# Kernel optimization log

Hardware: AMD Instinct MI355X
Metric: run time of the kernel (lower is better)

## Reference

```python
import math
import jax, jax.numpy as jnp
import numpy as np

B, N, W, D, H = 16, 64, 128, 128, 4

def posenc(L, d):
    pos = jnp.arange(L, dtype=jnp.float32)[:, None]
    div = jnp.exp(jnp.arange(0, d, 2, dtype=jnp.float32) * (-math.log(10000.0) / d))
    pe = jnp.zeros((L, d), jnp.float32)
    pe = pe.at[:, 0::2].set(jnp.sin(pos * div))
    pe = pe.at[:, 1::2].set(jnp.cos(pos * div))
    return pe

def ln(x):
    # torch nn.LayerNorm(x.shape[1:]) created fresh each call: normalize over all non-batch dims, no affine
    ax = tuple(range(1, x.ndim))
    m = x.mean(ax, keepdims=True)
    v = ((x - m) ** 2).mean(ax, keepdims=True)
    return (x - m) / jnp.sqrt(v + 1e-5)

def conv1d(x, w, b):
    # x [B,C,L], w [Cout,Cin,K] (torch layout), VALID padding
    y = jax.lax.conv_general_dilated(x, w, (1,), 'VALID', dimension_numbers=('NCH', 'OIH', 'NCH'))
    return y + b[None, :, None]

def convt1d(x, w, b, stride, pad):
    # torch ConvTranspose1d, w [Cin,Cout,K]
    K = w.shape[2]
    w_ = jnp.flip(w, 2).transpose(1, 0, 2)  # [Cout,Cin,K]
    y = jax.lax.conv_general_dilated(x, w_, (1,), [(K - 1 - pad, K - 1 - pad)],
                                     lhs_dilation=(stride,), dimension_numbers=('NCH', 'OIH', 'NCH'))
    return y + b[None, :, None]

def mha(q, k, v, wi, bi, wo, bo):
    # torch nn.MultiheadAttention(batch_first=True), H heads
    d = q.shape[-1]
    qp = q @ wi[:d].T + bi[:d]
    kp = k @ wi[d:2 * d].T + bi[d:2 * d]
    vp = v @ wi[2 * d:].T + bi[2 * d:]
    def heads(t):
        b_, l_, _ = t.shape
        return t.reshape(b_, l_, H, d // H).transpose(0, 2, 1, 3)
    qh, kh, vh = heads(qp), heads(kp), heads(vp)
    s = jnp.einsum('bhqd,bhkd->bhqk', qh, kh) / jnp.sqrt(jnp.asarray(d // H, qh.dtype))
    o = jnp.einsum('bhqk,bhkd->bhqd', jax.nn.softmax(s, -1), vh)
    b_, l_ = q.shape[0], q.shape[1]
    return o.transpose(0, 2, 1, 3).reshape(b_, l_, d) @ wo.T + bo


def setup_inputs():
    key = jax.random.key(0)
    ks = iter(jax.random.split(key, 64))
    def w(shape, s=0.05):
        return jax.random.normal(next(ks), shape, jnp.float32) * s
    inp = {}
    inp['tokens'] = jax.random.randint(next(ks), (B, N, W), 0, 257, jnp.int32)
    inp['emb_table'] = w((257, D), 1.0)
    for nm in ['ce', 'ct', 'cg', 'ces', 'cts']:
        inp['w_' + nm] = w((D, D, 3))
        inp['b_' + nm] = w((D,))
    inp['mha_wi'] = w((3 * D, D)); inp['mha_bi'] = w((3 * D,))
    inp['mha_wo'] = w((D, D)); inp['mha_bo'] = w((D,))
    s = 1.0 / math.sqrt(D)
    inp['tgt1'] = jax.random.uniform(next(ks), (1, D), jnp.float32, -s, s)
    inp['tgt2'] = jax.random.uniform(next(ks), (1, D), jnp.float32, -s, s)
    for nm in ['mu', 'lv', 'di']:
        inp['w_' + nm] = w((D, D)); inp['b_' + nm] = w((D,))
    inp['eps'] = jax.random.normal(next(ks), (B, D), jnp.float32)
    inp['dk_w'] = w((32, 32)); inp['dk_b'] = w((32,))
    inp['dv_w'] = w((32, 32)); inp['dv_b'] = w((32,))
    inp['wt1'] = w((32, 64, 3)); inp['bt1'] = w((64,))
    inp['wt2'] = w((64, 128, 3)); inp['bt2'] = w((128,))
    for nm in ['sq', 'sk', 'sv']:
        inp[nm + '_w'] = w((128, 128)); inp[nm + '_b'] = w((128,))
    inp['wt3'] = w((128, 128, 3)); inp['bt3'] = w((128,))
    return inp


def reference(tokens, emb_table, w_ce, b_ce, w_ct, b_ct, w_cg, b_cg, w_ces, b_ces, w_cts, b_cts,
              mha_wi, mha_bi, mha_wo, mha_bo, tgt1, tgt2,
              w_mu, b_mu, w_lv, b_lv, w_di, b_di, eps,
              dk_w, dk_b, dv_w, dv_b, wt1, bt1, wt2, bt2,
              sq_w, sq_b, sk_w, sk_b, sv_w, sv_b, wt3, bt3):
    emb = emb_table[tokens] + posenc(W, D)                    # [B,N,W,D]
    flat = emb.reshape(B * N, W, D)                           # batch the per-sample torch loop

    def word_branch(wc, bc, act):
        h = act(conv1d(flat.transpose(0, 2, 1), wc, bc)).transpose(0, 2, 1)  # [BN,W-2,D]
        return mha(h, h, h, mha_wi, mha_bi, mha_wo, mha_bo)

    a_e = jax.nn.elu(word_branch(w_ce, b_ce, jax.nn.elu))
    a_t = jnp.tanh(word_branch(w_ct, b_ct, jnp.tanh))
    xw = ln((a_e * a_t).reshape(B, N, W - 2, D)).reshape(B * N, W - 2, D)

    h = jax.nn.elu(conv1d(xw.transpose(0, 2, 1), w_cg, b_cg)).transpose(0, 2, 1)  # [BN,W-4,D]
    q1 = jnp.broadcast_to(tgt1[None], (B * N, 1, D))
    out = mha(q1, h, h, mha_wi, mha_bi, mha_wo, mha_bo)[:, 0, :].reshape(B, N, D)

    se = out + posenc(N, D)                                   # sentence level

    def sent_branch(wc, bc, act):
        hh = act(conv1d(se.transpose(0, 2, 1), wc, bc)).transpose(0, 2, 1)       # [B,N-2,D]
        return mha(hh, hh, hh, mha_wi, mha_bi, mha_wo, mha_bo)

    s_e = jax.nn.elu(sent_branch(w_ces, b_ces, jax.nn.elu))
    s_t = jnp.tanh(sent_branch(w_cts, b_cts, jnp.tanh))
    xs = ln(s_e * s_t)
    q2 = jnp.broadcast_to(tgt2[None], (B, 1, D))
    doc = mha(q2, xs, xs, mha_wi, mha_bi, mha_wo, mha_bo)[:, 0, :]

    mu = doc @ w_mu.T + b_mu
    lv = doc @ w_lv.T + b_lv
    z = mu + eps * jnp.exp(0.5 * lv)

    h = (z @ w_di.T + b_di).reshape(B, 32, -1)                # [B,32,4]
    L = h.shape[2]
    k = jnp.einsum('oi,bil->bol', dk_w, h) + dk_b[None, :, None]
    v = jnp.einsum('oi,bil->bol', dv_w, h) + dv_b[None, :, None]
    kh = k.reshape(B, H, 8, L)
    vh = v.reshape(B, H, 8, L)
    att = jax.nn.softmax(jnp.einsum('bhdl,bhdm->bhlm', kh, vh) / jnp.sqrt(8.0), -1)
    h = jax.nn.elu(jnp.einsum('bhlm,bhdm->bhld', att, vh).reshape(B, 32, L))
    h = jax.nn.elu(ln(convt1d(h, wt1, bt1, 2, 1)))            # [B,64,7]
    h = jax.nn.elu(ln(convt1d(h, wt2, bt2, 2, 1)))            # [B,128,13]
    L2 = h.shape[2]
    qc = jnp.einsum('oi,bil->bol', sq_w, h) + sq_b[None, :, None]
    kc = jnp.einsum('oi,bil->bol', sk_w, h) + sk_b[None, :, None]
    vc = jnp.einsum('oi,bil->bol', sv_w, h) + sv_b[None, :, None]
    qh = qc.reshape(B, H, 32, L2)
    khh = kc.reshape(B, H, 32, L2)
    att = jax.nn.softmax(jnp.einsum('bhdl,bhdm->bhlm', qh, khh) / jnp.sqrt(32.0), -1)
    vr = vc.reshape(B, H, 32, L2).reshape(B, H, L2, 32)       # faithful torch .view reinterpretation
    h = jax.nn.elu(jnp.einsum('bhlm,bhmd->bhld', att, vr).reshape(B, 128, L2))
    recon = jax.nn.sigmoid(ln(convt1d(h, wt3, bt3, 1, 1)))    # [B,128,13]
    return recon, mu, lv
```

## Files before the change

### kernel.cpp

```cpp
#include <hip/hip_runtime.h>
#include <hip/hip_bf16.h>

typedef __hip_bfloat16 bf16;
typedef __attribute__((ext_vector_type(8))) short bf16x8;
typedef __attribute__((ext_vector_type(4))) float f32x4;

__device__ __forceinline__ float b2f(bf16 x){ return __bfloat162float(x); }
__device__ __forceinline__ bf16  f2b(float x){ return __float2bfloat16(x); }
__device__ __forceinline__ unsigned short b2u(bf16 x){ union{bf16 b; unsigned short u;} c; c.b = x; return c.u; }

#define LOG2E 1.4426950408889634f
#define QSC (0.17677669529663687f * LOG2E)

#define GLD16(gp, lp) __builtin_amdgcn_global_load_lds( \
    (const __attribute__((address_space(1))) void*)(gp), \
    (__attribute__((address_space(3))) void*)(lp), 16, 0, 0)

__device__ __forceinline__ float fexp2(float x){
  float r; asm("v_exp_f32 %0, %1" : "=v"(r) : "v"(x)); return r;
}
__device__ __forceinline__ float fast_exp(float x){ return fexp2(x * LOG2E); }
__device__ __forceinline__ float eluf(float x){ return x > 0.f ? x : fast_exp(x) - 1.f; }
__device__ __forceinline__ float fast_tanh(float x){
  float cx = fminf(fmaxf(x, -15.f), 15.f);
  float t = fexp2(cx * (2.f*LOG2E));
  return (t - 1.f) / (t + 1.f);
}

#define PE_C (-0.07195578415606394f)

__device__ __forceinline__ float pe_val(int pos, int d){
  int j2 = d & ~1;
  float ang = (float)pos * expf((float)j2 * PE_C);
  return (d & 1) ? cosf(ang) : sinf(ang);
}

__device__ __forceinline__ void pack_one(const float* __restrict__ W, bf16* __restrict__ out,
                                         int K, int N, int conv, int qscale, int t){
  int j = t & 7, lane = (t >> 3) & 63;
  int rest = t >> 9; int NT = N >> 4;
  int nt = rest % NT; int kb = rest / NT;
  int k = kb*32 + ((lane >> 4) << 3) + j;
  int n = nt*16 + (lane & 15);
  float v = conv ? W[n*384 + (k & 127)*3 + (k >> 7)] : W[(long)n*K + k];
  if (qscale && n < 128) v *= QSC;
  out[t] = f2b(v);
}

__global__ void k_prep(const float* __restrict__ w_ce, const float* __restrict__ w_ct,
                       const float* __restrict__ w_cg, const float* __restrict__ w_ces,
                       const float* __restrict__ w_cts, const float* __restrict__ wi,
                       const float* __restrict__ wo,
                       bf16* P_CE, bf16* P_CT, bf16* P_CG, bf16* P_CES, bf16* P_CTS,
                       bf16* P_WI, bf16* P_WO, float* __restrict__ pet){
  int bid = blockIdx.x;
  if (bid < 1152){
    int grp = bid / 192; int t = (bid % 192)*256 + threadIdx.x;
    const float* W; bf16* out; int K, N, conv, qs = 0;
    if      (grp == 0){ W = w_ce;  out = P_CE;  K=384; N=128; conv=1; }
    else if (grp == 1){ W = w_ct;  out = P_CT;  K=384; N=128; conv=1; }
    else if (grp == 2){ W = w_cg;  out = P_CG;  K=384; N=128; conv=1; }
    else if (grp == 3){ W = w_ces; out = P_CES; K=384; N=128; conv=1; }
    else if (grp == 4){ W = w_cts; out = P_CTS; K=384; N=128; conv=1; }
    else              { W = wi;    out = P_WI;  K=128; N=384; conv=0; qs=1; }
    pack_one(W, out, K, N, conv, qs, t);
  } else if (bid < 1216){
    int t = (bid - 1152)*256 + threadIdx.x;
    pack_one(wo, P_WO, 128, 128, 0, 0, t);
  } else {
    int i = (bid - 1216)*256 + threadIdx.x;
    if (i < 16384) pet[i] = pe_val(i >> 7, i & 127);
  }
}

__global__ void k_qprep(const float* __restrict__ wi, const float* __restrict__ bi,
                        const float* __restrict__ t1, const float* __restrict__ t2,
                        float* __restrict__ rkv){
  int tid = threadIdx.x;
  __shared__ float qps[256];
  {
    int which = tid >> 7, jj = tid & 127;
    const float* t = which ? t2 : t1;
    float a = bi[jj];
    for (int i = 0; i < 128; ++i) a += wi[jj*128 + i] * t[i];
    qps[tid] = a;
  }
  __syncthreads();
  int i = tid & 127, which = tid >> 7;
  for (int h = 0; h < 4; ++h){
    float a = 0.f;
    for (int d = 0; d < 32; ++d) a += qps[which*128 + h*32 + d] * wi[(128 + h*32 + d)*128 + i];
    rkv[which*512 + h*128 + i] = a;
  }
}

template<bool GLL>
__global__ __launch_bounds__(256)
void k_gemm_mfma(const bf16* __restrict__ A, const bf16* __restrict__ Bp_, const bf16* __restrict__ Bp2,
                 const float* __restrict__ bias_, const float* __restrict__ bias2,
                 bf16* __restrict__ C_, bf16* __restrict__ C2p,
                 const bf16* __restrict__ mul,
                 int M, int K, int a_lout, int a_lind, int lda,
                 int NT, int n0t, int ldc, int act_, int act2,
                 const float* __restrict__ lnst, int lngrp,
                 const int* __restrict__ tok, const float* __restrict__ tabp,
                 const float* __restrict__ petp, const float* __restrict__ sepe,
                 float* __restrict__ part){
  const bf16* Bp = Bp_; const float* bias = bias_; bf16* C = C_; int act = act_;
  if (blockIdx.z){ Bp = Bp2; bias = bias2; C = C2p; act = act2; }

  __shared__ f32x4 AsV[2][512];
  __shared__ float redp[16];
  char* As0 = (char*)AsV[0];
  char* As1 = (char*)AsV[1];
  int tid = threadIdx.x;
  int lane = tid & 63, wave = tid >> 6;
  int wm = wave >> 1, wn = wave & 1;
  int m0 = blockIdx.x*128;
  int by = blockIdx.y;

  long offA[2]; bool okA[2]; float lnm[2], lnr[2]; int sbyte[2];
  #pragma unroll
  for (int p = 0; p < 2; ++p){
    int e = tid + p*256;
    int row, kq;
    if (GLL){
      int x = e;
      row = (((x >> 3) << 1) | (((x >> 2) ^ (x >> 4)) & 1)) & 127;
      kq  = ((((x >> 1) ^ (x >> 3)) & 1) << 1) | ((x ^ (x >> 2) ^ (x >> 4)) & 1);
    } else {
      row = e >> 2; kq = e & 3;
    }
    int m = m0 + row;
    okA[p] = (m < M);
    long off = 0;
    if (okA[p]){
      off = (a_lout > 0) ? (long)(m / a_lout)*a_lind + (long)(m % a_lout)*128 + kq*8
                         : (long)m*lda + kq*8;
    }
    offA[p] = off;
    lnm[p] = 0.f; lnr[p] = 1.f;
    if (!GLL && lnst && okA[p]){ int g = (int)(off / (long)lngrp); lnm[p] = lnst[2*g]; lnr[p] = lnst[2*g+1]; }
    sbyte[p] = (row*64 + kq*16) ^ ((row & 7) << 4);
  }

  const bf16* bptr[4];
  size_t bstep = (size_t)NT*512;
  #pragma unroll
  for (int fn = 0; fn < 4; ++fn){
    int ntile = n0t + by*8 + wn*4 + fn;
    bptr[fn] = Bp + ((size_t)ntile*64 + lane)*8;
  }
  int abyte[4];
  #pragma unroll
  for (int fm = 0; fm < 4; ++fm){
    int row = wm*64 + fm*16 + (lane & 15);
    abyte[fm] = (row*64 + ((lane >> 4) << 4)) ^ ((row & 7) << 4);
  }

  f32x4 acc[4][4];
  #pragma unroll
  for (int i = 0; i < 4; ++i)
    #pragma unroll
    for (int j = 0; j < 4; ++j) acc[i][j] = (f32x4){0.f,0.f,0.f,0.f};

  int nk = K >> 5;

  if constexpr (GLL){
    int ldsw = (tid >> 6)*1024;
    #pragma unroll
    for (int p = 0; p < 2; ++p)
      GLD16(A + offA[p], As0 + p*4096 + ldsw);
    __syncthreads();
    for (int kb = 0; kb < nk; ++kb){
      char* cur = (kb & 1) ? As1 : As0;
      char* nxt = (kb & 1) ? As0 : As1;
      bool more = (kb + 1) < nk;
      if (more){
        #pragma unroll
        for (int p = 0; p < 2; ++p)
          GLD16(A + offA[p] + (kb+1)*32, nxt + p*4096 + ldsw);
      }
      bf16x8 bfr[4];
      #pragma unroll
      for (int fn = 0; fn < 4; ++fn) bfr[fn] = *(const bf16x8*)(bptr[fn] + (size_t)kb*bstep);
      bf16x8 afr[4];
      #pragma unroll
      for (int fm = 0; fm < 4; ++fm) afr[fm] = *(const bf16x8*)(cur + abyte[fm]);
      #pragma unroll
      for (int fm = 0; fm < 4; ++fm)
        #pragma unroll
        for (int fn = 0; fn < 4; ++fn)
          acc[fm][fn] = __builtin_amdgcn_mfma_f32_16x16x32_bf16(afr[fm], bfr[fn], acc[fm][fn], 0, 0, 0);
      __syncthreads();
    }
  } else {
    auto loadA = [&](int p, int kb)->float4{
      float4 v = make_float4(0.f,0.f,0.f,0.f);
      if (okA[p]){
        long e = offA[p] + kb*32;
        if (tok){
          int seq = (int)(e >> 14); int rest = (int)e & 16383;
          int wrow = rest >> 7, d0 = rest & 127;
          int t = tok[(seq << 7) + wrow];
          const float* ta = tabp + t*128 + d0;
          const float* pe = petp + (wrow << 7) + d0;
          bf16 oo[8];
          #pragma unroll
          for (int u = 0; u < 8; ++u) oo[u] = f2b(ta[u] + pe[u]);
          v = *(float4*)&oo[0];
        } else {
          v = *(const float4*)(A + e);
          if (lnst){
            bf16* pp = (bf16*)&v; bf16 oo[8];
            #pragma unroll
            for (int u = 0; u < 8; ++u) oo[u] = f2b((b2f(pp[u]) - lnm[p]) * lnr[p]);
            v = *(float4*)&oo[0];
          }
        }
      }
      return v;
    };
    float4 va0 = loadA(0, 0), va1 = loadA(1, 0);
    *(float4*)(As0 + sbyte[0]) = va0;
    *(float4*)(As0 + sbyte[1]) = va1;
    __syncthreads();
    for (int kb = 0; kb < nk; ++kb){
      char* cur = (kb & 1) ? As1 : As0;
      char* nxt = (kb & 1) ? As0 : As1;
      bool more = (kb + 1) < nk;
      if (more){ va0 = loadA(0, kb+1); va1 = loadA(1, kb+1); }
      bf16x8 bfr[4];
      #pragma unroll
      for (int fn = 0; fn < 4; ++fn) bfr[fn] = *(const bf16x8*)(bptr[fn] + (size_t)kb*bstep);
      bf16x8 afr[4];
      #pragma unroll
      for (int fm = 0; fm < 4; ++fm) afr[fm] = *(const bf16x8*)(cur + abyte[fm]);
      #pragma unroll
      for (int fm = 0; fm < 4; ++fm)
        #pragma unroll
        for (int fn = 0; fn < 4; ++fn)
          acc[fm][fn] = __builtin_amdgcn_mfma_f32_16x16x32_bf16(afr[fm], bfr[fn], acc[fm][fn], 0, 0, 0);
      if (more){
        *(float4*)(nxt + sbyte[0]) = va0;
        *(float4*)(nxt + sbyte[1]) = va1;
      }
      __syncthreads();
    }
  }

  float ps = 0.f, ps2 = 0.f;
  #pragma unroll
  for (int fm = 0; fm < 4; ++fm){
    #pragma unroll
    for (int r = 0; r < 4; ++r){
      int m = m0 + wm*64 + fm*16 + ((lane >> 4) << 2) + r;
      if (m >= M) continue;
      #pragma unroll
      for (int fn = 0; fn < 4; ++fn){
        int n = by*128 + wn*64 + fn*16 + (lane & 15);
        float v = acc[fm][fn][r] + (bias ? bias[n] : 0.f);
        if (act == 1) v = eluf(v);
        else if (act == 2) v = fast_tanh(v);
        if (mul) v *= b2f(mul[(long)m*ldc + n]);
        if (sepe) v += sepe[(m & 63)*128 + n];
        if (part){ ps += v; ps2 += v*v; }
        C[(long)m*ldc + n] = f2b(v);
      }
    }
  }
  if (part){
    #pragma unroll
    for (int o = 32; o; o >>= 1){ ps += __shfl_xor(ps, o); ps2 += __shfl_xor(ps2, o); }
    if (lane == 0){ redp[wave] = ps; redp[8 + wave] = ps2; }
    __syncthreads();
    if (tid == 0){
      part[blockIdx.x*2]     = redp[0]+redp[1]+redp[2]+redp[3];
      part[blockIdx.x*2 + 1] = redp[8]+redp[9]+redp[10]+redp[11];
    }
  }
}

template<int L>
__global__ __launch_bounds__(256)
void k_attn_fused(const bf16* __restrict__ X, const bf16* __restrict__ Pwi,
                  const float* __restrict__ bi, bf16* __restrict__ o){
  constexpr int KB  = (L + 31) / 32;
  constexpr int MT  = KB * 2;
  constexpr int WMT = MT / 4;
  constexpr int NP  = KB * 32;
  constexpr int PRS = NP * 2;

  __shared__ alignas(16) char As[NP*256];
  __shared__ alignas(16) char Qb[NP*64];
  __shared__ alignas(16) char Kb[NP*64];
  __shared__ alignas(16) char Vt[32*PRS];
  char* Pb = As;

  int tid = threadIdx.x;
  int s = blockIdx.x >> 2, h = blockIdx.x & 3;
  const bf16* xb = X + (size_t)s*L*128;

  {
    constexpr int NCH = (NP*16)/256;
    int ldsw = (tid >> 6)*1024;
    #pragma unroll
    for (int p = 0; p < NCH; ++p){
      int x = p*256 + tid;
      int row = x >> 4;
      int c = (x & 15) ^ (row & 7);
      const bf16* gp = (row < L) ? (xb + (size_t)row*128 + c*8) : xb;
      GLD16(gp, As + p*4096 + ldsw);
    }
  }
  __syncthreads();

  int lane = tid & 63, wave = tid >> 6;
  int col = lane & 15;

  __builtin_amdgcn_s_setprio(1);
  #pragma unroll
  for (int mt = 0; mt < WMT; ++mt){
    int mtile = wave*WMT + mt;
    int arow = mtile*16 + col;
    bf16x8 a4[4];
    #pragma unroll
    for (int kb = 0; kb < 4; ++kb)
      a4[kb] = *(const bf16x8*)(As + ((arow*256 + kb*64 + ((lane >> 4) << 4)) ^ ((arow & 7) << 4)));
    #pragma unroll
    for (int which = 0; which < 3; ++which){
      f32x4 av[2];
      #pragma unroll
      for (int nt = 0; nt < 2; ++nt){
        int ntile = which*8 + h*2 + nt;
        float bia = bi[which*128 + h*32 + nt*16 + col];
        if (which == 0) bia *= QSC;
        av[nt] = (f32x4){bia, bia, bia, bia};
        #pragma unroll
        for (int kb = 0; kb < 4; ++kb){
          bf16x8 bfr = *(const bf16x8*)(Pwi + (((size_t)kb*24 + ntile)*64 + lane)*8);
          av[nt] = __builtin_amdgcn_mfma_f32_16x16x32_bf16(a4[kb], bfr, av[nt], 0, 0, 0);
        }
      }
      #pragma unroll
      for (int r = 0; r < 4; ++r){
        int row = mtile*16 + ((lane >> 4) << 2) + r;
        if (which < 2){
          unsigned pk = (unsigned)b2u(f2b(av[0][r])) | ((unsigned)b2u(f2b(av[1][r])) << 16);
          char* dst = which ? Kb : Qb;
          *(unsigned*)(dst + ((row*64 + col*4) ^ ((row & 7) << 4))) = pk;
        } else {
          int pos = (row & 15)*MT + (row >> 4);
          #pragma unroll
          for (int nt = 0; nt < 2; ++nt){
            int d = nt*16 + col;
            *(bf16*)(Vt + ((d*PRS + pos*2) ^ ((d & 7) << 4))) = f2b(av[nt][r]);
          }
        }
      }
    }
  }
  __builtin_amdgcn_s_setprio(0);
  __syncthreads();

  f32x4 acc[WMT][MT];
  #pragma unroll
  for (int mt = 0; mt < WMT; ++mt)
    #pragma unroll
    for (int nt = 0; nt < MT; ++nt) acc[mt][nt] = (f32x4){0.f,0.f,0.f,0.f};

  bf16x8 af[WMT];
  #pragma unroll
  for (int mt = 0; mt < WMT; ++mt){
    int row = (wave*WMT + mt)*16 + col;
    af[mt] = *(const bf16x8*)(Qb + ((row*64 + ((lane >> 4) << 4)) ^ ((row & 7) << 4)));
  }
  __builtin_amdgcn_s_setprio(1);
  #pragma unroll
  for (int nt = 0; nt < MT; ++nt){
    int rk2 = nt*16 + col;
    bf16x8 bfk = *(const bf16x8*)(Kb + ((rk2*64 + ((lane >> 4) << 4)) ^ ((rk2 & 7) << 4)));
    #pragma unroll
    for (int mt = 0; mt < WMT; ++mt)
      acc[mt][nt] = __builtin_amdgcn_mfma_f32_16x16x32_bf16(af[mt], bfk, acc[mt][nt], 0, 0, 0);
  }
  __builtin_amdgcn_s_setprio(0);

  const bool lastMask = col >= (L - (MT-1)*16);
  float pinv[WMT][4];
  #pragma unroll
  for (int mt = 0; mt < WMT; ++mt){
    #pragma unroll
    for (int r = 0; r < 4; ++r){
      float mx = -1e30f;
      #pragma unroll
      for (int nt = 0; nt < MT; ++nt){
        float v = acc[mt][nt][r];
        if (nt == MT-1 && lastMask){ v = -1e30f; acc[mt][nt][r] = v; }
        mx = fmaxf(mx, v);
      }
      mx = fmaxf(mx, __shfl_xor(mx, 1));
      mx = fmaxf(mx, __shfl_xor(mx, 2));
      mx = fmaxf(mx, __shfl_xor(mx, 4));
      mx = fmaxf(mx, __shfl_xor(mx, 8));
      float sum = 0.f;
      bf16 prow[MT];
      #pragma unroll
      for (int nt = 0; nt < MT; ++nt){
        float p = fexp2(acc[mt][nt][r] - mx);
        prow[nt] = f2b(p);
        sum += p;
      }
      sum += __shfl_xor(sum, 1);
      sum += __shfl_xor(sum, 2);
      sum += __shfl_xor(sum, 4);
      sum += __shfl_xor(sum, 8);
      pinv[mt][r] = 1.f / sum;
      int row = (wave*WMT + mt)*16 + ((lane >> 4) << 2) + r;
      char* dst = Pb + ((row*PRS + col*(MT*2)) ^ ((row & 7) << 4));
      if constexpr (MT == 8) *(f32x4*)dst = *(f32x4*)prow;
      else                   *(float2*)dst = *(float2*)prow;
    }
  }

  #pragma unroll
  for (int mt = 0; mt < WMT; ++mt){
    int mtile = wave*WMT + mt;
    f32x4 o0 = (f32x4){0.f,0.f,0.f,0.f}, o1 = (f32x4){0.f,0.f,0.f,0.f};
    __builtin_amdgcn_s_setprio(1);
    #pragma unroll
    for (int kb = 0; kb < KB; ++kb){
      int row = mtile*16 + col;
      bf16x8 pa = *(const bf16x8*)(Pb + ((row*PRS + kb*64 + ((lane >> 4) << 4)) ^ ((row & 7) << 4)));
      int d0 = col;
      bf16x8 v0 = *(const bf16x8*)(Vt + ((d0*PRS + kb*64 + ((lane >> 4) << 4)) ^ ((d0 & 7) << 4)));
      bf16x8 v1 = *(const bf16x8*)(Vt + (((d0+16)*PRS + kb*64 + ((lane >> 4) << 4)) ^ (((d0+16) & 7) << 4)));
      o0 = __builtin_amdgcn_mfma_f32_16x16x32_bf16(pa, v0, o0, 0, 0, 0);
      o1 = __builtin_amdgcn_mfma_f32_16x16x32_bf16(pa, v1, o1, 0, 0, 0);
    }
    __builtin_amdgcn_s_setprio(0);
    #pragma unroll
    for (int r = 0; r < 4; ++r){
      int row = mtile*16 + ((lane >> 4) << 2) + r;
      if (row < L){
        size_t ob = ((size_t)s*L + row)*128 + h*32 + col;
        o[ob]      = f2b(o0[r] * pinv[mt][r]);
        o[ob + 16] = f2b(o1[r] * pinv[mt][r]);
      }
    }
  }
}

template<int L>
__global__ __launch_bounds__(256)
void k_attn_tgt(const bf16* __restrict__ hin, const float* __restrict__ rk,
                const float* __restrict__ wi, const float* __restrict__ bi,
                bf16* __restrict__ outp){
  __shared__ alignas(16) char Hs[L*256];
  __shared__ float RKs[512];
  __shared__ float Ps[512];
  __shared__ float Cs[512];
  int tid = threadIdx.x, lane = tid & 63, wave = tid >> 6;
  int s = blockIdx.x;
  const bf16* hb = hin + (size_t)s*L*128;
  for (int e = tid; e < L*16; e += 256){
    int row = e >> 4, c = e & 15;
    *(float4*)(Hs + row*256 + ((c ^ (row & 7)) << 4)) = *(const float4*)(hb + row*128 + c*8);
  }
  for (int e = tid; e < 512; e += 256) RKs[e] = rk[e];
  __syncthreads();

  int j0 = lane, j1 = lane + 64;
  float v0 = -1e30f, v1 = -1e30f;
  if (j0 < L){
    float a = 0.f;
    #pragma unroll
    for (int c = 0; c < 16; ++c){
      bf16x8 x = *(const bf16x8*)(Hs + j0*256 + ((c ^ (j0 & 7)) << 4));
      #pragma unroll
      for (int u = 0; u < 8; ++u) a += b2f(((bf16*)&x)[u]) * RKs[wave*128 + c*8 + u];
    }
    v0 = a * 0.17677669529663687f;
  }
  if (j1 < L){
    float a = 0.f;
    #pragma unroll
    for (int c = 0; c < 16; ++c){
      bf16x8 x = *(const bf16x8*)(Hs + j1*256 + ((c ^ (j1 & 7)) << 4));
      #pragma unroll
      for (int u = 0; u < 8; ++u) a += b2f(((bf16*)&x)[u]) * RKs[wave*128 + c*8 + u];
    }
    v1 = a * 0.17677669529663687f;
  }
  float mx = fmaxf(v0, v1);
  #pragma unroll
  for (int off = 32; off; off >>= 1) mx = fmaxf(mx, __shfl_xor(mx, off));
  float e0 = (j0 < L) ? fast_exp(v0 - mx) : 0.f;
  float e1 = (j1 < L) ? fast_exp(v1 - mx) : 0.f;
  float sum = e0 + e1;
  #pragma unroll
  for (int off = 32; off; off >>= 1) sum += __shfl_xor(sum, off);
  float inv = 1.f / sum;
  Ps[wave*128 + j0] = e0 * inv;
  Ps[wave*128 + j1] = e1 * inv;

  int i0 = lane*2;
  float c0 = 0.f, c1 = 0.f;
  for (int j = 0; j < L; ++j){
    float p = Ps[wave*128 + j];
    short2 w2 = *(const short2*)(Hs + j*256 + (((i0 >> 3) ^ (j & 7)) << 4) + (i0 & 7)*2);
    c0 += p * b2f(*(bf16*)&w2.x);
    c1 += p * b2f(*(bf16*)&w2.y);
  }
  Cs[wave*128 + i0]     = c0;
  Cs[wave*128 + i0 + 1] = c1;
  __syncthreads();

  if (tid < 128){
    int h2 = tid >> 5;
    float a = bi[256 + tid];
    const float* wr = wi + (size_t)(256 + tid)*128;
    for (int i = 0; i < 128; ++i) a += wr[i] * Cs[h2*128 + i];
    outp[(size_t)s*128 + tid] = f2b(a);
  }
}

__global__ void k_ln_fin(const float* __restrict__ part, float* __restrict__ stats, int P, int GS){
  int g = blockIdx.x;
  float s = 0.f, s2 = 0.f;
  for (int i = threadIdx.x; i < P; i += 256){ s += part[(g*P + i)*2]; s2 += part[(g*P + i)*2 + 1]; }
  #pragma unroll
  for (int off = 32; off; off >>= 1){ s += __shfl_xor(s, off); s2 += __shfl_xor(s2, off); }
  __shared__ float sh[8];
  int lane = threadIdx.x & 63, wv = threadIdx.x >> 6;
  if (lane == 0){ sh[wv] = s; sh[4 + wv] = s2; }
  __syncthreads();
  if (threadIdx.x == 0){
    float S = sh[0]+sh[1]+sh[2]+sh[3], S2 = sh[4]+sh[5]+sh[6]+sh[7];
    float mean = S / GS;
    float var = S2 / GS - mean*mean;
    stats[g*2] = mean; stats[g*2 + 1] = rsqrtf(var + 1e-5f);
  }
}

__global__ void k_ln_small_bf16(const bf16* __restrict__ x, bf16* __restrict__ y, int n){
  int g = blockIdx.x;
  const bf16* xb = x + (size_t)g*n;
  bf16* yb = y + (size_t)g*n;
  float s = 0.f, s2 = 0.f;
  for (int i = threadIdx.x; i < n; i += 256){ float v = b2f(xb[i]); s += v; s2 += v*v; }
  #pragma unroll
  for (int off = 32; off; off >>= 1){ s += __shfl_xor(s, off); s2 += __shfl_xor(s2, off); }
  __shared__ float sh[8];  __shared__ float ms[2];
  int lane = threadIdx.x & 63, wv = threadIdx.x >> 6;
  if (lane == 0){ sh[wv] = s; sh[4 + wv] = s2; }
  __syncthreads();
  if (threadIdx.x == 0){
    float S = sh[0]+sh[1]+sh[2]+sh[3], S2 = sh[4]+sh[5]+sh[6]+sh[7];
    float mean = S / n;
    ms[0] = mean; ms[1] = rsqrtf(S2 / n - mean*mean + 1e-5f);
  }
  __syncthreads();
  float mean = ms[0], inv = ms[1];
  for (int i = threadIdx.x; i < n; i += 256) yb[i] = f2b((b2f(xb[i]) - mean)*inv);
}

__global__ void k_ln_small_f32(const float* __restrict__ x, float* __restrict__ y, int n, int act){
  int g = blockIdx.x;
  const float* xb = x + (size_t)g*n;
  float* yb = y + (size_t)g*n;
  float s = 0.f, s2 = 0.f;
  for (int i = threadIdx.x; i < n; i += 256){ float v = xb[i]; s += v; s2 += v*v; }
  #pragma unroll
  for (int off = 32; off; off >>= 1){ s += __shfl_xor(s, off); s2 += __shfl_xor(s2, off); }
  __shared__ float sh[8];  __shared__ float ms[2];
  int lane = threadIdx.x & 63, wv = threadIdx.x >> 6;
  if (lane == 0){ sh[wv] = s; sh[4 + wv] = s2; }
  __syncthreads();
  if (threadIdx.x == 0){
    float S = sh[0]+sh[1]+sh[2]+sh[3], S2 = sh[4]+sh[5]+sh[6]+sh[7];
    float mean = S / n;
    ms[0] = mean; ms[1] = rsqrtf(S2 / n - mean*mean + 1e-5f);
  }
  __syncthreads();
  float mean = ms[0], inv = ms[1];
  for (int i = threadIdx.x; i < n; i += 256){
    float v = (xb[i] - mean)*inv;
    if (act == 1) v = eluf(v);
    else if (act == 3) v = 1.f/(1.f + fast_exp(-v));
    yb[i] = v;
  }
}

__global__ __launch_bounds__(256)
void k_dec_a(const bf16* __restrict__ DOC,
             const float* __restrict__ w_mu, const float* __restrict__ b_mu,
             const float* __restrict__ w_lv, const float* __restrict__ b_lv,
             const float* __restrict__ eps,
             const float* __restrict__ w_di, const float* __restrict__ b_di,
             const float* __restrict__ dk_w, const float* __restrict__ dk_b,
             const float* __restrict__ dv_w, const float* __restrict__ dv_b,
             const float* __restrict__ wt1, const float* __restrict__ bt1,
             float* __restrict__ dout, float* __restrict__ DEC2){
  int b = blockIdx.x, tid = threadIdx.x;
  __shared__ float Zs[128], H3[128], KD[128], VD[128], D1[128];
  __shared__ float C1[448];
  __shared__ float sc[64];
  __shared__ float red[8], ms[2];

  if (tid < 128){
    const bf16* dr = DOC + b*128;
    float mu = b_mu[tid], lv = b_lv[tid];
    for (int i = 0; i < 128; ++i){
      float x = b2f(dr[i]);
      mu += x * w_mu[tid*128 + i];
      lv += x * w_lv[tid*128 + i];
    }
    dout[26624 + b*128 + tid] = mu;
    dout[28672 + b*128 + tid] = lv;
    Zs[tid] = mu + eps[b*128 + tid] * fast_exp(0.5f*lv);
  }
  __syncthreads();
  if (tid < 128){
    float a = b_di[tid];
    for (int i = 0; i < 128; ++i) a += Zs[i] * w_di[tid*128 + i];
    H3[tid] = a;
  }
  __syncthreads();
  if (tid < 128){
    int l = tid & 3, o2 = tid >> 2;
    float ak = dk_b[o2], av = dv_b[o2];
    for (int i = 0; i < 32; ++i){
      float xv = H3[i*4 + l];
      ak += dk_w[o2*32 + i]*xv;
      av += dv_w[o2*32 + i]*xv;
    }
    KD[tid] = ak; VD[tid] = av;
  }
  __syncthreads();
  if (tid < 64){
    int h = tid >> 4, l = (tid >> 2) & 3, m = tid & 3;
    float a = 0.f;
    #pragma unroll
    for (int d = 0; d < 8; ++d) a += KD[(h*8+d)*4 + l] * VD[(h*8+d)*4 + m];
    sc[tid] = a * 0.35355339059327373f;
  }
  __syncthreads();
  if (tid < 16){
    int base = tid*4;
    float mx = fmaxf(fmaxf(sc[base],sc[base+1]),fmaxf(sc[base+2],sc[base+3]));
    float e0=fast_exp(sc[base]-mx), e1=fast_exp(sc[base+1]-mx), e2=fast_exp(sc[base+2]-mx), e3=fast_exp(sc[base+3]-mx);
    float inv = 1.f/(e0+e1+e2+e3);
    sc[base]=e0*inv; sc[base+1]=e1*inv; sc[base+2]=e2*inv; sc[base+3]=e3*inv;
  }
  __syncthreads();
  if (tid < 128){
    int h = tid >> 5, rem = tid & 31, l = rem >> 3, d = rem & 7;
    float a = 0.f;
    #pragma unroll
    for (int m = 0; m < 4; ++m) a += sc[h*16 + l*4 + m] * VD[(h*8+d)*4 + m];
    D1[tid] = eluf(a);
  }
  __syncthreads();
  for (int idx = tid; idx < 448; idx += 256){
    int co = idx / 7, lo = idx % 7;
    float a = bt1[co];
    for (int k = 0; k < 3; ++k){
      int t = lo + 1 - k;
      if (t < 0 || (t & 1)) continue;
      int li = t >> 1; if (li >= 4) continue;
      float aa = 0.f;
      for (int ci = 0; ci < 32; ++ci) aa += D1[ci*4 + li] * wt1[ci*192 + co*3 + k];
      a += aa;
    }
    C1[idx] = a;
  }
  __syncthreads();
  {
    float s = 0.f, s2 = 0.f;
    for (int i = tid; i < 448; i += 256){ float v = C1[i]; s += v; s2 += v*v; }
    #pragma unroll
    for (int o = 32; o; o >>= 1){ s += __shfl_xor(s, o); s2 += __shfl_xor(s2, o); }
    int lane = tid & 63, wv = tid >> 6;
    if (lane == 0){ red[wv] = s; red[4+wv] = s2; }
    __syncthreads();
    if (tid == 0){
      float S = red[0]+red[1]+red[2]+red[3], S2 = red[4]+red[5]+red[6]+red[7];
      float mean = S/448.f; ms[0] = mean; ms[1] = rsqrtf(S2/448.f - mean*mean + 1e-5f);
    }
    __syncthreads();
    float mean = ms[0], inv = ms[1];
    for (int i = tid; i < 448; i += 256)
      DEC2[b*448 + i] = eluf((C1[i]-mean)*inv);
  }
}

__global__ void k_chanproj3(const float* __restrict__ x,
                            const float* __restrict__ w1, const float* __restrict__ b1,
                            const float* __restrict__ w2, const float* __restrict__ b2,
                            const float* __restrict__ w3, const float* __restrict__ b3,
                            float* __restrict__ y1, float* __restrict__ y2, float* __restrict__ y3,
                            int Bn, int C, int L){
  int idx = blockIdx.x*256 + threadIdx.x;
  if (idx >= Bn*C*L) return;
  int l = idx % L; int t2 = idx / L; int o = t2 % C; int b = t2 / C;
  float a1 = b1[o], a2 = b2[o], a3 = b3[o];
  const float* xb = x + (size_t)b*C*L + l;
  for (int i = 0; i < C; ++i){
    float xv = xb[i*L];
    a1 += w1[(size_t)o*C + i]*xv;
    a2 += w2[(size_t)o*C + i]*xv;
    a3 += w3[(size_t)o*C + i]*xv;
  }
  y1[idx] = a1; y2[idx] = a2; y3[idx] = a3;
}

__global__ __launch_bounds__(256)
void k_dec_attn2(const float* __restrict__ qc, const float* __restrict__ kc,
                 const float* __restrict__ vc, float* __restrict__ out){
  int b = blockIdx.x >> 2, h = blockIdx.x & 3, tid = threadIdx.x;
  __shared__ float sc[169];
  const float* qb = qc + b*1664 + h*416;
  const float* kb = kc + b*1664 + h*416;
  const float* vb = vc + b*1664 + h*416;
  if (tid < 169){
    int l = tid/13, m = tid - l*13;
    float a = 0.f;
    #pragma unroll
    for (int d = 0; d < 32; ++d) a += qb[d*13 + l] * kb[d*13 + m];
    sc[tid] = a * 0.17677669529663687f;
  }
  __syncthreads();
  if (tid < 13){
    float mx = -1e30f;
    for (int m = 0; m < 13; ++m) mx = fmaxf(mx, sc[tid*13 + m]);
    float s = 0.f;
    for (int m = 0; m < 13; ++m){ float p = fast_exp(sc[tid*13 + m] - mx); sc[tid*13 + m] = p; s += p; }
    float inv = 1.f/s;
    for (int m = 0; m < 13; ++m) sc[tid*13 + m] *= inv;
  }
  __syncthreads();
  for (int idx = tid; idx < 416; idx += 256){
    int l = idx >> 5, d = idx & 31;
    float a = 0.f;
    for (int m = 0; m < 13; ++m) a += sc[l*13 + m] * vb[m*32 + d];
    out[b*1664 + h*416 + idx] = eluf(a);
  }
}

__global__ __launch_bounds__(256)
void k_convt(const float* __restrict__ x, const float* __restrict__ w,
             const float* __restrict__ bias, float* __restrict__ y,
             int Bn, int Ci, int Co, int Lin, int Lout, int stride, int pad, int nch){
  __shared__ float xs[1664];
  int b = blockIdx.x / nch;
  int c0 = (blockIdx.x % nch)*16;
  int tid = threadIdx.x;
  for (int i = tid; i < Ci*Lin; i += 256) xs[i] = x[(size_t)b*Ci*Lin + i];
  __syncthreads();
  int co = c0 + (tid & 15);
  int lo = tid >> 4;
  if (co >= Co || lo >= Lout) return;
  float a = bias[co];
  for (int k = 0; k < 3; ++k){
    int t = lo + pad - k;
    if (t < 0 || (t % stride)) continue;
    int li = t / stride;
    if (li >= Lin) continue;
    float aa = 0.f;
    for (int ci = 0; ci < Ci; ++ci) aa += xs[ci*Lin + li] * w[(size_t)ci*Co*3 + co*3 + k];
    a += aa;
  }
  y[(size_t)b*Co*Lout + co*Lout + lo] = a;
}

extern "C" void kernel_launch(void* const* d_in, const int* in_sizes, int n_in,
                              void* d_out, int out_size, void* d_ws, size_t ws_size,
                              hipStream_t stream){
  const int*   tokens = (const int*)  d_in[0];
  const float* tab    = (const float*)d_in[1];
  const float* w_ce = (const float*)d_in[2];  const float* b_ce = (const float*)d_in[3];
  const float* w_ct = (const float*)d_in[4];  const float* b_ct = (const float*)d_in[5];
  const float* w_cg = (const float*)d_in[6];  const float* b_cg = (const float*)d_in[7];
  const float* w_ces= (const float*)d_in[8];  const float* b_ces= (const float*)d_in[9];
  const float* w_cts= (const float*)d_in[10]; const float* b_cts= (const float*)d_in[11];
  const float* wi   = (const float*)d_in[12]; const float* bi   = (const float*)d_in[13];
  const float* wo   = (const float*)d_in[14]; const float* bo   = (const float*)d_in[15];
  const float* tgt1 = (const float*)d_in[16]; const float* tgt2 = (const float*)d_in[17];
  const float* w_mu = (const float*)d_in[18]; const float* b_mu = (const float*)d_in[19];
  const float* w_lv = (const float*)d_in[20]; const float* b_lv = (const float*)d_in[21];
  const float* w_di = (const float*)d_in[22]; const float* b_di = (const float*)d_in[23];
  const float* epsb = (const float*)d_in[24];
  const float* dk_w = (const float*)d_in[25]; const float* dk_b = (const float*)d_in[26];
  const float* dv_w = (const float*)d_in[27]; const float* dv_b = (const float*)d_in[28];
  const float* wt1  = (const float*)d_in[29]; const float* bt1  = (const float*)d_in[30];
  const float* wt2  = (const float*)d_in[31]; const float* bt2  = (const float*)d_in[32];
  const float* sq_w = (const float*)d_in[33]; const float* sq_b = (const float*)d_in[34];
  const float* sk_w = (const float*)d_in[35]; const float* sk_b = (const float*)d_in[36];
  const float* sv_w = (const float*)d_in[37]; const float* sv_b = (const float*)d_in[38];
  const float* wt3  = (const float*)d_in[39]; const float* bt3  = (const float*)d_in[40];

  float* dout = (float*)d_out;

  char* ws = (char*)d_ws;
  size_t off = 0;
  auto take = [&](size_t bytes)->char*{ char* p = ws + off; off += (bytes + 255) & ~(size_t)255; return p; };
  bf16* EMB  = (bf16*)take(16777216ull*2);
  bf16* HB   = (bf16*)take(16515072ull*2);
  bf16* OB   = (bf16*)take(16515072ull*2);
  bf16* AE   = (bf16*)take(16515072ull*2);
  bf16* O1   = (bf16*)take(131072ull*2);
  bf16* SEB  = (bf16*)take(131072ull*2);
  bf16* SH   = (bf16*)take(126976ull*2);
  bf16* SCT  = (bf16*)take(126976ull*2);
  bf16* SO   = (bf16*)take(126976ull*2);
  bf16* SAE  = (bf16*)take(126976ull*2);
  bf16* XS   = (bf16*)take(126976ull*2);
  bf16* DO1  = (bf16*)take(2048ull*2);
  bf16* DOC  = (bf16*)take(2048ull*2);
  float* RK  = (float*)take(1024*4);
  float* PART= (float*)take(1008ull*2*4);
  float* STATS=(float*)take(32*4);
  float* DEC2= (float*)take(7168*4);
  float* C2  = (float*)take(26624*4);
  float* DEC3= (float*)take(26624*4);
  float* QC  = (float*)take(26624*4);
  float* KC  = (float*)take(26624*4);
  float* VC  = (float*)take(26624*4);
  float* DEC4= (float*)take(26624*4);
  float* C3  = (float*)take(26624*4);
  float* PET = (float*)take(16384*4);
  bf16* P_CE = (bf16*)take(49152ull*2);
  bf16* P_CT = (bf16*)take(49152ull*2);
  bf16* P_CG = (bf16*)take(49152ull*2);
  bf16* P_CES= (bf16*)take(49152ull*2);
  bf16* P_CTS= (bf16*)take(49152ull*2);
  bf16* P_WI = (bf16*)take(49152ull*2);
  bf16* P_WO = (bf16*)take(16384ull*2);
  (void)ws_size; (void)in_sizes; (void)n_in; (void)out_size;

  auto cdiv = [](long a, long b){ return (int)((a + b - 1)/b); };
  auto gemm = [&](const bf16* A, const bf16* Bpp, const float* bias, bf16* C, const bf16* mul,
                  int M, int N, int K, int a_lout, int a_lind, int lda, int NT, int n0t, int ldc, int act,
                  const float* lnst, int lngrp, const float* sepe, float* part){
    dim3 g(cdiv(M,128), N/128, 1);
    if (lnst)
      k_gemm_mfma<false><<<g, 256, 0, stream>>>(A, Bpp, Bpp, bias, bias, C, C, mul,
                                                M, K, a_lout, a_lind, lda, NT, n0t, ldc, act, act, lnst, lngrp,
                                                nullptr, nullptr, nullptr, sepe, part);
    else
      k_gemm_mfma<true><<<g, 256, 0, stream>>>(A, Bpp, Bpp, bias, bias, C, C, mul,
                                               M, K, a_lout, a_lind, lda, NT, n0t, ldc, act, act, nullptr, 0,
                                               nullptr, nullptr, nullptr, sepe, part);
  };
  auto gemmz_emb = [&](const bf16* Bp1, const float* b1, bf16* C1, int act1,
                       const bf16* Bp2, const float* b2, bf16* C2p, int act2,
                       int M, int N, int K, int a_lout, int a_lind, int NT, int ldc){
    dim3 g(cdiv(M,128), N/128, 2);
    k_gemm_mfma<false><<<g, 256, 0, stream>>>(nullptr, Bp1, Bp2, b1, b2, C1, C2p, nullptr,
                                              M, K, a_lout, a_lind, 0, NT, 0, ldc, act1, act2, nullptr, 0,
                                              tokens, tab, PET, nullptr, nullptr);
  };
  auto gemmz = [&](const bf16* A, const bf16* Bp1, const float* b1, bf16* C1, int act1,
                   const bf16* Bp2, const float* b2, bf16* C2p, int act2,
                   int M, int N, int K, int a_lout, int a_lind, int lda, int NT, int n0t, int ldc){
    dim3 g(cdiv(M,128), N/128, 2);
    k_gemm_mfma<true><<<g, 256, 0, stream>>>(A, Bp1, Bp2, b1, b2, C1, C2p, nullptr,
                                             M, K, a_lout, a_lind, lda, NT, n0t, ldc, act1, act2, nullptr, 0,
                                             nullptr, nullptr, nullptr, nullptr, nullptr);
  };

  k_prep<<<1280, 256, 0, stream>>>(w_ce, w_ct, w_cg, w_ces, w_cts, wi, wo,
                                   P_CE, P_CT, P_CG, P_CES, P_CTS, P_WI, P_WO, PET);
  k_qprep<<<1, 256, 0, stream>>>(wi, bi, tgt1, tgt2, RK);

  gemmz_emb(P_CE, b_ce, HB, 1, P_CT, b_ct, OB, 2, 129024, 128, 384, 126, 16384, 8, 128);

  k_attn_fused<126><<<4096, 256, 0, stream>>>(HB, P_WI, bi, EMB);
  gemm(EMB, P_WO, bo, AE, nullptr, 129024, 128, 128, 0, 0, 128, 8, 0, 128, 1, nullptr, 0, nullptr, nullptr);

  k_attn_fused<126><<<4096, 256, 0, stream>>>(OB, P_WI, bi, EMB);
  gemm(EMB, P_WO, bo, HB, AE, 129024, 128, 128, 0, 0, 128, 8, 0, 128, 2, nullptr, 0, nullptr, PART);

  k_ln_fin<<<16, 256, 0, stream>>>(PART, STATS, 63, 1032192);

  gemm(HB, P_CG, b_cg, OB, nullptr, 126976, 128, 384, 124, 16128, 0, 8, 0, 128, 1, STATS, 1032192, nullptr, nullptr);

  k_attn_tgt<124><<<1024, 256, 0, stream>>>(OB, RK, wi, bi, O1);
  gemm(O1, P_WO, bo, SEB, nullptr, 1024, 128, 128, 0, 0, 128, 8, 0, 128, 0, nullptr, 0, PET, nullptr);

  gemmz(SEB, P_CES, b_ces, SH, 1, P_CTS, b_cts, SCT, 2, 992, 128, 384, 62, 8192, 0, 8, 0, 128);

  k_attn_fused<62><<<64, 256, 0, stream>>>(SH, P_WI, bi, SO);
  gemm(SO, P_WO, bo, SAE, nullptr, 992, 128, 128, 0, 0, 128, 8, 0, 128, 1, nullptr, 0, nullptr, nullptr);

  k_attn_fused<62><<<64, 256, 0, stream>>>(SCT, P_WI, bi, SO);
  gemm(SO, P_WO, bo, SH, SAE, 992, 128, 128, 0, 0, 128, 8, 0, 128, 2, nullptr, 0, nullptr, nullptr);

  k_ln_small_bf16<<<16, 256, 0, stream>>>(SH, XS, 7936);

  k_attn_tgt<62><<<16, 256, 0, stream>>>(XS, RK + 512, wi, bi, DO1);
  gemm(DO1, P_WO, bo, DOC, nullptr, 16, 128, 128, 0, 0, 128, 8, 0, 128, 0, nullptr, 0, nullptr, nullptr);

  k_dec_a<<<16, 256, 0, stream>>>(DOC, w_mu, b_mu, w_lv, b_lv, epsb, w_di, b_di,
                                  dk_w, dk_b, dv_w, dv_b, wt1, bt1, dout, DEC2);
  k_convt<<<16*8, 256, 0, stream>>>(DEC2, wt2, bt2, C2, 16, 64, 128, 7, 13, 2, 1, 8);
  k_ln_small_f32<<<16, 256, 0, stream>>>(C2, DEC3, 1664, 1);
  k_chanproj3<<<cdiv(26624,256), 256, 0, stream>>>(DEC3, sq_w, sq_b, sk_w, sk_b, sv_w, sv_b,
                                                   QC, KC, VC, 16, 128, 13);
  k_dec_attn2<<<64, 256, 0, stream>>>(QC, KC, VC, DEC4);
  k_convt<<<16*8, 256, 0, stream>>>(DEC4, wt3, bt3, C3, 16, 128, 128, 13, 13, 1, 1, 8);
  k_ln_small_f32<<<16, 256, 0, stream>>>(C3, dout, 1664, 3);
}
```

Measured before the change: 668.7 us.

## Materialize embeddings separately and deepen GLL GEMM K-tile to 64

The token-embedding plus positional-encoding gather moves out of the first conv GEMM into a standalone kernel that writes bf16 embeddings to a buffer. That GEMM then runs through the async global-to-LDS path instead of the register-staged gather path. The GLL GEMM now stages 64-wide K slices per barrier, with a new XOR swizzle and doubled LDS, which halves the number of syncs per tile. The cost is an extra pass that writes and rereads the embedding tensor, plus higher LDS use that may reduce occupancy.

```diff
diff --git a/kernel.cpp b/kernel.cpp
--- a/kernel.cpp
+++ b/kernel.cpp
@@ -94,6 +94,20 @@
   }
 }
 
+__global__ void k_embed8(const int* __restrict__ tok, const float* __restrict__ tab,
+                         const float* __restrict__ pet, bf16* __restrict__ out){
+  int t = blockIdx.x*256 + threadIdx.x;
+  int q = t & 15;
+  int flat = t >> 4; int w = flat & 127;
+  int tk = tok[flat];
+  const float* ta = tab + tk*128 + q*8;
+  const float* pe = pet + (w << 7) + q*8;
+  bf16 ob[8];
+  #pragma unroll
+  for (int i = 0; i < 8; ++i) ob[i] = f2b(ta[i] + pe[i]);
+  *(f32x4*)(out + (size_t)t*8) = *(f32x4*)ob;
+}
+
 template<bool GLL>
 __global__ __launch_bounds__(256)
 void k_gemm_mfma(const bf16* __restrict__ A, const bf16* __restrict__ Bp_, const bf16* __restrict__ Bp2,
@@ -103,13 +117,11 @@
                  int M, int K, int a_lout, int a_lind, int lda,
                  int NT, int n0t, int ldc, int act_, int act2,
                  const float* __restrict__ lnst, int lngrp,
-                 const int* __restrict__ tok, const float* __restrict__ tabp,
-                 const float* __restrict__ petp, const float* __restrict__ sepe,
-                 float* __restrict__ part){
+                 const float* __restrict__ sepe, float* __restrict__ part){
   const bf16* Bp = Bp_; const float* bias = bias_; bf16* C = C_; int act = act_;
   if (blockIdx.z){ Bp = Bp2; bias = bias2; C = C2p; act = act2; }
 
-  __shared__ f32x4 AsV[2][512];
+  __shared__ f32x4 AsV[2][1024];
   __shared__ float redp[16];
   char* As0 = (char*)AsV[0];
   char* As1 = (char*)AsV[1];
@@ -119,31 +131,6 @@
   int m0 = blockIdx.x*128;
   int by = blockIdx.y;
 
-  long offA[2]; bool okA[2]; float lnm[2], lnr[2]; int sbyte[2];
-  #pragma unroll
-  for (int p = 0; p < 2; ++p){
-    int e = tid + p*256;
-    int row, kq;
-    if (GLL){
-      int x = e;
-      row = (((x >> 3) << 1) | (((x >> 2) ^ (x >> 4)) & 1)) & 127;
-      kq  = ((((x >> 1) ^ (x >> 3)) & 1) << 1) | ((x ^ (x >> 2) ^ (x >> 4)) & 1);
-    } else {
-      row = e >> 2; kq = e & 3;
-    }
-    int m = m0 + row;
-    okA[p] = (m < M);
-    long off = 0;
-    if (okA[p]){
-      off = (a_lout > 0) ? (long)(m / a_lout)*a_lind + (long)(m % a_lout)*128 + kq*8
-                         : (long)m*lda + kq*8;
-    }
-    offA[p] = off;
-    lnm[p] = 0.f; lnr[p] = 1.f;
-    if (!GLL && lnst && okA[p]){ int g = (int)(off / (long)lngrp); lnm[p] = lnst[2*g]; lnr[p] = lnst[2*g+1]; }
-    sbyte[p] = (row*64 + kq*16) ^ ((row & 7) << 4);
-  }
-
   const bf16* bptr[4];
   size_t bstep = (size_t)NT*512;
   #pragma unroll
@@ -151,12 +138,6 @@
     int ntile = n0t + by*8 + wn*4 + fn;
     bptr[fn] = Bp + ((size_t)ntile*64 + lane)*8;
   }
-  int abyte[4];
-  #pragma unroll
-  for (int fm = 0; fm < 4; ++fm){
-    int row = wm*64 + fm*16 + (lane & 15);
-    abyte[fm] = (row*64 + ((lane >> 4) << 4)) ^ ((row & 7) << 4);
-  }
 
   f32x4 acc[4][4];
   #pragma unroll
@@ -164,63 +145,96 @@
     #pragma unroll
     for (int j = 0; j < 4; ++j) acc[i][j] = (f32x4){0.f,0.f,0.f,0.f};
 
-  int nk = K >> 5;
-
   if constexpr (GLL){
-    int ldsw = (tid >> 6)*1024;
-    #pragma unroll
-    for (int p = 0; p < 2; ++p)
-      GLD16(A + offA[p], As0 + p*4096 + ldsw);
+    long offA4[4];
+    #pragma unroll
+    for (int p = 0; p < 4; ++p){
+      int x = p*256 + tid;
+      int row = x >> 3;
+      int kq = (x & 7) ^ (row & 7);
+      int m = m0 + row;
+      long off = 0;
+      if (m < M)
+        off = (a_lout > 0) ? (long)(m / a_lout)*a_lind + (long)(m % a_lout)*128 + kq*8
+                           : (long)m*lda + kq*8;
+      offA4[p] = off;
+    }
+    int abyte[4];
+    #pragma unroll
+    for (int fm = 0; fm < 4; ++fm){
+      int row = wm*64 + fm*16 + (lane & 15);
+      abyte[fm] = row*128 + ((((lane >> 4) ^ (row & 7)) & 7) << 4);
+    }
+    int ldsw = wave*1024;
+    int nt64 = K >> 6;
+    #pragma unroll
+    for (int p = 0; p < 4; ++p)
+      GLD16(A + offA4[p], As0 + p*4096 + ldsw);
     __syncthreads();
-    for (int kb = 0; kb < nk; ++kb){
-      char* cur = (kb & 1) ? As1 : As0;
-      char* nxt = (kb & 1) ? As0 : As1;
-      bool more = (kb + 1) < nk;
-      if (more){
+    for (int t = 0; t < nt64; ++t){
+      char* cur = (t & 1) ? As1 : As0;
+      char* nxt = (t & 1) ? As0 : As1;
+      if (t + 1 < nt64){
         #pragma unroll
-        for (int p = 0; p < 2; ++p)
-          GLD16(A + offA[p] + (kb+1)*32, nxt + p*4096 + ldsw);
-      }
-      bf16x8 bfr[4];
-      #pragma unroll
-      for (int fn = 0; fn < 4; ++fn) bfr[fn] = *(const bf16x8*)(bptr[fn] + (size_t)kb*bstep);
-      bf16x8 afr[4];
-      #pragma unroll
-      for (int fm = 0; fm < 4; ++fm) afr[fm] = *(const bf16x8*)(cur + abyte[fm]);
-      #pragma unroll
-      for (int fm = 0; fm < 4; ++fm)
+        for (int p = 0; p < 4; ++p)
+          GLD16(A + offA4[p] + (t+1)*64, nxt + p*4096 + ldsw);
+      }
+      #pragma unroll
+      for (int sub = 0; sub < 2; ++sub){
+        int kb = t*2 + sub;
+        bf16x8 bfr[4];
         #pragma unroll
-        for (int fn = 0; fn < 4; ++fn)
-          acc[fm][fn] = __builtin_amdgcn_mfma_f32_16x16x32_bf16(afr[fm], bfr[fn], acc[fm][fn], 0, 0, 0);
+        for (int fn = 0; fn < 4; ++fn) bfr[fn] = *(const bf16x8*)(bptr[fn] + (size_t)kb*bstep);
+        bf16x8 afr[4];
+        #pragma unroll
+        for (int fm = 0; fm < 4; ++fm)
+          afr[fm] = *(const bf16x8*)(cur + (abyte[fm] ^ (sub << 6)));
+        #pragma unroll
+        for (int fm = 0; fm < 4; ++fm)
+          #pragma unroll
+          for (int fn = 0; fn < 4; ++fn)
+            acc[fm][fn] = __builtin_amdgcn_mfma_f32_16x16x32_bf16(afr[fm], bfr[fn], acc[fm][fn], 0, 0, 0);
+      }
       __syncthreads();
     }
   } else {
+    long offA[2]; bool okA[2]; float lnm[2], lnr[2]; int sbyte[2];
+    #pragma unroll
+    for (int p = 0; p < 2; ++p){
+      int e = tid + p*256;
+      int row = e >> 2, kq = e & 3;
+      int m = m0 + row;
+      okA[p] = (m < M);
+      long off = 0;
+      if (okA[p]){
+        off = (a_lout > 0) ? (long)(m / a_lout)*a_lind + (long)(m % a_lout)*128 + kq*8
+                           : (long)m*lda + kq*8;
+      }
+      offA[p] = off;
+      lnm[p] = 0.f; lnr[p] = 1.f;
+      if (lnst && okA[p]){ int g = (int)(off / (long)lngrp); lnm[p] = lnst[2*g]; lnr[p] = lnst[2*g+1]; }
+      sbyte[p] = (row*64 + kq*16) ^ ((row & 7) << 4);
+    }
+    int abyte[4];
+    #pragma unroll
+    for (int fm = 0; fm < 4; ++fm){
+      int row = wm*64 + fm*16 + (lane & 15);
+      abyte[fm] = (row*64 + ((lane >> 4) << 4)) ^ ((row & 7) << 4);
+    }
     auto loadA = [&](int p, int kb)->float4{
       float4 v = make_float4(0.f,0.f,0.f,0.f);
       if (okA[p]){
-        long e = offA[p] + kb*32;
-        if (tok){
-          int seq = (int)(e >> 14); int rest = (int)e & 16383;
-          int wrow = rest >> 7, d0 = rest & 127;
-          int t = tok[(seq << 7) + wrow];
-          const float* ta = tabp + t*128 + d0;
-          const float* pe = petp + (wrow << 7) + d0;
-          bf16 oo[8];
+        v = *(const float4*)(A + offA[p] + kb*32);
+        if (lnst){
+          bf16* pp = (bf16*)&v; bf16 oo[8];
           #pragma unroll
-          for (int u = 0; u < 8; ++u) oo[u] = f2b(ta[u] + pe[u]);
+          for (int u = 0; u < 8; ++u) oo[u] = f2b((b2f(pp[u]) - lnm[p]) * lnr[p]);
           v = *(float4*)&oo[0];
-        } else {
-          v = *(const float4*)(A + e);
-          if (lnst){
-            bf16* pp = (bf16*)&v; bf16 oo[8];
-            #pragma unroll
-            for (int u = 0; u < 8; ++u) oo[u] = f2b((b2f(pp[u]) - lnm[p]) * lnr[p]);
-            v = *(float4*)&oo[0];
-          }
         }
       }
       return v;
     };
+    int nk = K >> 5;
     float4 va0 = loadA(0, 0), va1 = loadA(1, 0);
     *(float4*)(As0 + sbyte[0]) = va0;
     *(float4*)(As0 + sbyte[1]) = va1;
@@ -847,19 +861,11 @@
     if (lnst)
       k_gemm_mfma<false><<<g, 256, 0, stream>>>(A, Bpp, Bpp, bias, bias, C, C, mul,
                                                 M, K, a_lout, a_lind, lda, NT, n0t, ldc, act, act, lnst, lngrp,
-                                                nullptr, nullptr, nullptr, sepe, part);
+                                                sepe, part);
     else
       k_gemm_mfma<true><<<g, 256, 0, stream>>>(A, Bpp, Bpp, bias, bias, C, C, mul,
                                                M, K, a_lout, a_lind, lda, NT, n0t, ldc, act, act, nullptr, 0,
-                                               nullptr, nullptr, nullptr, sepe, part);
-  };
-  auto gemmz_emb = [&](const bf16* Bp1, const float* b1, bf16* C1, int act1,
-                       const bf16* Bp2, const float* b2, bf16* C2p, int act2,
-                       int M, int N, int K, int a_lout, int a_lind, int NT, int ldc){
-    dim3 g(cdiv(M,128), N/128, 2);
-    k_gemm_mfma<false><<<g, 256, 0, stream>>>(nullptr, Bp1, Bp2, b1, b2, C1, C2p, nullptr,
-                                              M, K, a_lout, a_lind, 0, NT, 0, ldc, act1, act2, nullptr, 0,
-                                              tokens, tab, PET, nullptr, nullptr);
+                                               sepe, part);
   };
   auto gemmz = [&](const bf16* A, const bf16* Bp1, const float* b1, bf16* C1, int act1,
                    const bf16* Bp2, const float* b2, bf16* C2p, int act2,
@@ -867,14 +873,15 @@
     dim3 g(cdiv(M,128), N/128, 2);
     k_gemm_mfma<true><<<g, 256, 0, stream>>>(A, Bp1, Bp2, b1, b2, C1, C2p, nullptr,
                                              M, K, a_lout, a_lind, lda, NT, n0t, ldc, act1, act2, nullptr, 0,
-                                             nullptr, nullptr, nullptr, nullptr, nullptr);
+                                             nullptr, nullptr);
   };
 
   k_prep<<<1280, 256, 0, stream>>>(w_ce, w_ct, w_cg, w_ces, w_cts, wi, wo,
                                    P_CE, P_CT, P_CG, P_CES, P_CTS, P_WI, P_WO, PET);
   k_qprep<<<1, 256, 0, stream>>>(wi, bi, tgt1, tgt2, RK);
-
-  gemmz_emb(P_CE, b_ce, HB, 1, P_CT, b_ct, OB, 2, 129024, 128, 384, 126, 16384, 8, 128);
+  k_embed8<<<8192, 256, 0, stream>>>(tokens, tab, PET, EMB);
+
+  gemmz(EMB, P_CE, b_ce, HB, 1, P_CT, b_ct, OB, 2, 129024, 128, 384, 126, 16384, 0, 8, 0, 128);
 
   k_attn_fused<126><<<4096, 256, 0, stream>>>(HB, P_WI, bi, EMB);
   gemm(EMB, P_WO, bo, AE, nullptr, 129024, 128, 128, 0, 0, 128, 8, 0, 128, 1, nullptr, 0, nullptr, nullptr);
```

New measurement: 655.6 us. 2.0% less time.
